# Kernel optimization log

Hardware: AMD Instinct MI355X
Metric: run time of the kernel (lower is better)

Reference implementation:

```python
import jax, jax.numpy as jnp
import numpy as np

B, S, DIM, H = 4, 4096, 2048, 16
HD = DIM // H  # head_dim = 128


def setup_inputs() -> dict:
    key = jax.random.key(0)
    ks = jax.random.split(key, 6)
    X = jax.random.normal(ks[0], (B, S, DIM), dtype=jnp.float32)
    freqs_cos = jax.random.uniform(ks[1], (S, HD), dtype=jnp.float32)
    freqs_sin = jax.random.uniform(ks[2], (S, HD), dtype=jnp.float32)
    attention_mask = jnp.ones((B, S), dtype=jnp.int32)
    # Linear weights stored as [in, out] (equivalent to torch W.T); no bias.
    scale = 0.02
    Wq = jax.random.normal(ks[3], (DIM, DIM), dtype=jnp.float32) * scale
    Wk = jax.random.normal(ks[4], (DIM, DIM), dtype=jnp.float32) * scale
    Wv = jax.random.normal(ks[5], (DIM, DIM), dtype=jnp.float32) * scale
    return {"X": X, "freqs_cos": freqs_cos, "freqs_sin": freqs_sin,
            "attention_mask": attention_mask, "Wq": Wq, "Wk": Wk, "Wv": Wv}


def _rotate_half_interleaved(x):
    # x: [B, S, H, D]; pairs along last dim: (x0, x1) -> (-x1, x0), interleaved
    xp = x.reshape(*x.shape[:-1], HD // 2, 2)
    xt = jnp.stack([-xp[..., 1], xp[..., 0]], axis=-1)
    return xt.reshape(x.shape)


def reference(X, freqs_cos, freqs_sin, attention_mask, Wq, Wk, Wv):
    bs, seq_len, _ = X.shape
    # QKV projections (no bias), fused view to [B, S, H, HD]
    Xq = (X @ Wq).reshape(bs, seq_len, H, HD)
    Xk = (X @ Wk).reshape(bs, seq_len, H, HD)
    Xv = (X @ Wv).reshape(bs, seq_len, H, HD)
    # RoPE: broadcast freqs to (1, S, 1, HD)
    cos = freqs_cos[None, :, None, :]
    sin = freqs_sin[None, :, None, :]
    Xq_out = Xq * cos + _rotate_half_interleaved(Xq) * sin
    Xk_out = Xk * cos + _rotate_half_interleaved(Xk) * sin
    return (Xq_out, Xk_out, Xv)
```

## Files before the change

kernel.cpp:

```cpp
#include <hip/hip_runtime.h>
#include <hip/hip_bf16.h>
#include <stdint.h>

#define B_    4
#define S_    4096
#define DIM_  2048
#define H_    16
#define HD_   128
#define M_    (B_ * S_)
#define K_    DIM_
#define N_    (3 * DIM_)

typedef __attribute__((ext_vector_type(8))) short bf16x8;
typedef __attribute__((ext_vector_type(4))) float f32x4;

__global__ void cvt_x_kernel(const float* __restrict__ X,
                             __hip_bfloat16* __restrict__ Xb) {
    size_t i = ((size_t)blockIdx.x * 256 + threadIdx.x) * 8;
    float4 a = *reinterpret_cast<const float4*>(X + i);
    float4 b = *reinterpret_cast<const float4*>(X + i + 4);
    union { __hip_bfloat16 h[8]; uint4 u; } o;
    o.h[0] = __float2bfloat16(a.x);
    o.h[1] = __float2bfloat16(a.y);
    o.h[2] = __float2bfloat16(a.z);
    o.h[3] = __float2bfloat16(a.w);
    o.h[4] = __float2bfloat16(b.x);
    o.h[5] = __float2bfloat16(b.y);
    o.h[6] = __float2bfloat16(b.z);
    o.h[7] = __float2bfloat16(b.w);
    *reinterpret_cast<uint4*>(Xb + i) = o.u;
}

__global__ void cvt_w_kernel(const float* __restrict__ Wq,
                             const float* __restrict__ Wk,
                             const float* __restrict__ Wv,
                             __hip_bfloat16* __restrict__ Wt) {
    __shared__ float tile[32][33];
    int w = blockIdx.z;
    const float* W = (w == 0) ? Wq : (w == 1) ? Wk : Wv;
    int n0 = blockIdx.x * 32;
    int k0 = blockIdx.y * 32;
    int tx = threadIdx.x, ty = threadIdx.y;
#pragma unroll
    for (int r = 0; r < 4; ++r) {
        int k = k0 + ty + r * 8;
        tile[ty + r * 8][tx] = W[(size_t)k * DIM_ + n0 + tx];
    }
    __syncthreads();
#pragma unroll
    for (int r = 0; r < 4; ++r) {
        int n = n0 + ty + r * 8;
        Wt[(size_t)(w * DIM_ + n) * K_ + k0 + tx] =
            __float2bfloat16(tile[tx][ty + r * 8]);
    }
}

#define BM 128
#define BN 256
#define BK 32
#define NT (K_ / BK)

#define BAR()      asm volatile("s_barrier" ::: "memory")
#define WAIT_VM(n) asm volatile("s_waitcnt vmcnt(" #n ")" ::: "memory")

__global__ __launch_bounds__(512, 4) void gemm_rope_kernel(
    const __hip_bfloat16* __restrict__ Xb,
    const __hip_bfloat16* __restrict__ Wt,
    const float* __restrict__ fcos,
    const float* __restrict__ fsin,
    float* __restrict__ out)
{
    __shared__ __hip_bfloat16 As[3][BM * BK];
    __shared__ __hip_bfloat16 Bs[3][BN * BK];

    int bid   = blockIdx.x;
    int x     = bid & 7;
    int local = bid >> 3;
    int tn = x * 3 + local % 3;
    int tm = local / 3;
    int m0 = tm * BM, n0 = tn * BN;

    int tid  = threadIdx.x;
    int lane = tid & 63;
    int w    = tid >> 6;
    int wr   = w >> 2;
    int wc   = w & 3;

    int srow = lane >> 2;
    int sgl  = lane & 3;
    int sgs  = (sgl ^ ((lane >> 3) & 3)) * 8;
    int sgd  = sgl * 8;

    int fr = lane & 15;
    int fq = lane >> 4;
    int fk = (fq ^ ((fr >> 1) & 3)) * 8;

#define STAGE_A(t, bb) do {                                                    \
        const __hip_bfloat16* _s = Xb + (size_t)(m0 + w * 16 + srow) * K_      \
                                      + (t) * BK + sgs;                        \
        __hip_bfloat16* _d = &As[bb][(w * 16 + srow) * BK + sgd];              \
        __builtin_amdgcn_global_load_lds(                                      \
            (const __attribute__((address_space(1))) void*)_s,                 \
            (__attribute__((address_space(3))) void*)_d, 16, 0, 0);            \
    } while (0)

#define STAGE_B(t, bb, r) do {                                                 \
        const __hip_bfloat16* _s = Wt + (size_t)(n0 + w * 32 + (r) * 16 + srow) * K_ \
                                      + (t) * BK + sgs;                        \
        __hip_bfloat16* _d = &Bs[bb][(w * 32 + (r) * 16 + srow) * BK + sgd];   \
        __builtin_amdgcn_global_load_lds(                                      \
            (const __attribute__((address_space(1))) void*)_s,                 \
            (__attribute__((address_space(3))) void*)_d, 16, 0, 0);            \
    } while (0)

    f32x4  acc[4][4] = {};
    bf16x8 a[4], b[4];

#define LDA(bb) do {                                                           \
        _Pragma("unroll")                                                      \
        for (int i = 0; i < 4; ++i)                                            \
            a[i] = *reinterpret_cast<const bf16x8*>(                           \
                &As[bb][(wr * 64 + i * 16 + fr) * BK + fk]);                   \
    } while (0)

#define LDB(bb) do {                                                           \
        _Pragma("unroll")                                                      \
        for (int j = 0; j < 4; ++j)                                            \
            b[j] = *reinterpret_cast<const bf16x8*>(                           \
                &Bs[bb][(wc * 64 + j * 16 + fr) * BK + fk]);                   \
    } while (0)

#define MFMA16() do {                                                          \
        __builtin_amdgcn_s_setprio(1);                                         \
        _Pragma("unroll")                                                      \
        for (int i = 0; i < 4; ++i)                                            \
        _Pragma("unroll")                                                      \
        for (int j = 0; j < 4; ++j)                                            \
            acc[i][j] = __builtin_amdgcn_mfma_f32_16x16x32_bf16(               \
                a[i], b[j], acc[i][j], 0, 0, 0);                               \
        __builtin_amdgcn_s_setprio(0);                                         \
    } while (0)

#define TILE(t, P, QS) do {                                                    \
        if ((t) + 2 < NT) {                                                    \
            STAGE_A((t) + 2, QS);                                              \
            STAGE_B((t) + 2, QS, 0); STAGE_B((t) + 2, QS, 1);                  \
        }                                                                      \
        LDA(P); LDB(P);                                                        \
        MFMA16();                                                              \
        if ((t) + 2 < NT) { WAIT_VM(3); } else { WAIT_VM(0); }                 \
        BAR();                                                                 \
    } while (0)

    STAGE_A(0, 0); STAGE_B(0, 0, 0); STAGE_B(0, 0, 1);
    STAGE_A(1, 1); STAGE_B(1, 1, 0); STAGE_B(1, 1, 1);
    WAIT_VM(3);
    BAR();

    for (int u = 0; u < (NT - 1) / 3; ++u) {
        TILE(3 * u + 0, 0, 2);
        TILE(3 * u + 1, 1, 0);
        TILE(3 * u + 2, 2, 1);
    }
    TILE(NT - 1, 0, 2);

#pragma unroll
    for (int i = 0; i < 4; ++i) {
        int mbase = m0 + wr * 64 + i * 16 + fq * 4;
#pragma unroll
        for (int j = 0; j < 4; ++j) {
            int n = n0 + wc * 64 + j * 16 + fr;
            int region = n >> 11;
            int cc = n & (DIM_ - 1);
            int d  = cc & (HD_ - 1);
#pragma unroll
            for (int r = 0; r < 4; ++r) {
                int m = mbase + r;
                int s = m & (S_ - 1);
                float g  = acc[i][j][r];
                float gp = __shfl_xor(g, 1, 64);
                float o;
                if (region < 2) {
                    float cv = fcos[s * HD_ + d];
                    float sv = fsin[s * HD_ + d];
                    o = g * cv + ((cc & 1) ? gp * sv : -gp * sv);
                } else {
                    o = g;
                }
                __builtin_nontemporal_store(
                    o, &out[(size_t)region * M_ * DIM_ + (size_t)m * DIM_ + cc]);
            }
        }
    }
#undef STAGE_A
#undef STAGE_B
#undef LDA
#undef LDB
#undef MFMA16
#undef TILE
}

extern "C" void kernel_launch(void* const* d_in, const int* in_sizes, int n_in,
                              void* d_out, int out_size, void* d_ws, size_t ws_size,
                              hipStream_t stream) {
    const float* X    = (const float*)d_in[0];
    const float* fcos = (const float*)d_in[1];
    const float* fsin = (const float*)d_in[2];
    const float* Wq   = (const float*)d_in[4];
    const float* Wk   = (const float*)d_in[5];
    const float* Wv   = (const float*)d_in[6];
    float* out = (float*)d_out;

    __hip_bfloat16* Xb  = (__hip_bfloat16*)d_ws;
    __hip_bfloat16* Wtp = Xb + (size_t)M_ * K_;

    {
        int threads = 256;
        int blocks = (M_ * K_) / (threads * 8);
        cvt_x_kernel<<<blocks, threads, 0, stream>>>(X, Xb);
    }
    {
        dim3 grid(DIM_ / 32, DIM_ / 32, 3);
        dim3 block(32, 8);
        cvt_w_kernel<<<grid, block, 0, stream>>>(Wq, Wk, Wv, Wtp);
    }
    {
        int blocks = (M_ / BM) * (N_ / BN);
        gemm_rope_kernel<<<blocks, 512, 0, stream>>>(Xb, Wtp, fcos, fsin, out);
    }
}
```

Baseline: 525.1 us.

## Deepen GEMM pipeline to four LDS stages with register double-buffered fragments

The main loop moves from three to four LDS buffers, prefetching three tiles ahead. The A/B fragments are now double-buffered in registers, so the LDS reads for the next tile are issued before the MFMAs on the current tile. The goal is to hide both global-load and LDS latency behind matrix math. In exchange, LDS use rises to 96KB and register pressure roughly doubles for fragments, so the launch bound drops to 2 blocks per CU, which lowers occupancy.

```diff
diff --git a/kernel.cpp b/kernel.cpp
--- a/kernel.cpp
+++ b/kernel.cpp
@@ -61,17 +61,18 @@
 #define NT (K_ / BK)
 
 #define BAR()      asm volatile("s_barrier" ::: "memory")
+#define LGKM0()    asm volatile("s_waitcnt lgkmcnt(0)" ::: "memory")
 #define WAIT_VM(n) asm volatile("s_waitcnt vmcnt(" #n ")" ::: "memory")
 
-__global__ __launch_bounds__(512, 4) void gemm_rope_kernel(
+__global__ __launch_bounds__(512, 2) void gemm_rope_kernel(
     const __hip_bfloat16* __restrict__ Xb,
     const __hip_bfloat16* __restrict__ Wt,
     const float* __restrict__ fcos,
     const float* __restrict__ fsin,
     float* __restrict__ out)
 {
-    __shared__ __hip_bfloat16 As[3][BM * BK];
-    __shared__ __hip_bfloat16 Bs[3][BN * BK];
+    __shared__ __hip_bfloat16 As[4][BM * BK];
+    __shared__ __hip_bfloat16 Bs[4][BN * BK];
 
     int bid   = blockIdx.x;
     int x     = bid & 7;
@@ -114,55 +115,66 @@
     } while (0)
 
     f32x4  acc[4][4] = {};
-    bf16x8 a[4], b[4];
-
-#define LDA(bb) do {                                                           \
+    bf16x8 aR[2][4], bR[2][4];
+
+#define LDA(rs, bb) do {                                                       \
         _Pragma("unroll")                                                      \
         for (int i = 0; i < 4; ++i)                                            \
-            a[i] = *reinterpret_cast<const bf16x8*>(                           \
+            aR[rs][i] = *reinterpret_cast<const bf16x8*>(                      \
                 &As[bb][(wr * 64 + i * 16 + fr) * BK + fk]);                   \
     } while (0)
 
-#define LDB(bb) do {                                                           \
+#define LDB(rs, bb) do {                                                       \
         _Pragma("unroll")                                                      \
         for (int j = 0; j < 4; ++j)                                            \
-            b[j] = *reinterpret_cast<const bf16x8*>(                           \
+            bR[rs][j] = *reinterpret_cast<const bf16x8*>(                      \
                 &Bs[bb][(wc * 64 + j * 16 + fr) * BK + fk]);                   \
     } while (0)
 
-#define MFMA16() do {                                                          \
+#define MFMA16(ms) do {                                                        \
         __builtin_amdgcn_s_setprio(1);                                         \
         _Pragma("unroll")                                                      \
         for (int i = 0; i < 4; ++i)                                            \
         _Pragma("unroll")                                                      \
         for (int j = 0; j < 4; ++j)                                            \
             acc[i][j] = __builtin_amdgcn_mfma_f32_16x16x32_bf16(               \
-                a[i], b[j], acc[i][j], 0, 0, 0);                               \
+                aR[ms][i], bR[ms][j], acc[i][j], 0, 0, 0);                     \
         __builtin_amdgcn_s_setprio(0);                                         \
     } while (0)
 
-#define TILE(t, P, QS) do {                                                    \
-        if ((t) + 2 < NT) {                                                    \
-            STAGE_A((t) + 2, QS);                                              \
-            STAGE_B((t) + 2, QS, 0); STAGE_B((t) + 2, QS, 1);                  \
-        }                                                                      \
-        LDA(P); LDB(P);                                                        \
-        MFMA16();                                                              \
-        if ((t) + 2 < NT) { WAIT_VM(3); } else { WAIT_VM(0); }                 \
+#define TILE(t, SBUF, RBUF, MS, RS) do {                                       \
+        STAGE_A((t) + 3, SBUF);                                                \
+        STAGE_B((t) + 3, SBUF, 0); STAGE_B((t) + 3, SBUF, 1);                  \
+        WAIT_VM(6);                                                            \
+        LGKM0();                                                               \
         BAR();                                                                 \
+        LDA(RS, RBUF); LDB(RS, RBUF);                                          \
+        MFMA16(MS);                                                            \
     } while (0)
 
     STAGE_A(0, 0); STAGE_B(0, 0, 0); STAGE_B(0, 0, 1);
     STAGE_A(1, 1); STAGE_B(1, 1, 0); STAGE_B(1, 1, 1);
-    WAIT_VM(3);
+    STAGE_A(2, 2); STAGE_B(2, 2, 0); STAGE_B(2, 2, 1);
+    WAIT_VM(6);
     BAR();
-
-    for (int u = 0; u < (NT - 1) / 3; ++u) {
-        TILE(3 * u + 0, 0, 2);
-        TILE(3 * u + 1, 1, 0);
-        TILE(3 * u + 2, 2, 1);
-    }
-    TILE(NT - 1, 0, 2);
+    LDA(0, 0); LDB(0, 0);
+
+    for (int u = 0; u < 15; ++u) {
+        int t = 4 * u;
+        TILE(t + 0, 3, 1, 0, 1);
+        TILE(t + 1, 0, 2, 1, 0);
+        TILE(t + 2, 1, 3, 0, 1);
+        TILE(t + 3, 2, 0, 1, 0);
+    }
+    TILE(60, 3, 1, 0, 1);
+    WAIT_VM(3); LGKM0(); BAR();
+    LDA(0, 2); LDB(0, 2);
+    MFMA16(1);
+    WAIT_VM(0); LGKM0(); BAR();
+    LDA(1, 3); LDB(1, 3);
+    MFMA16(0);
+    LGKM0(); BAR();
+    MFMA16(1);
 
 #pragma unroll
     for (int i = 0; i < 4; ++i) {
```

Result: slower. 595.3 us (+13.4%).
